# Kernel tuning notes

Hardware: AMD Instinct MI355X
Metric: run time of the kernel (lower is better)

Reference implementation:

```python
import jax, jax.numpy as jnp
import numpy as np
from jax import lax

B, T, D = 2, 2048, 2048
H, DK, DV = 16, 128, 128
K = 4  # conv kernel size
KEY_DIM = H * DK      # 2048
VAL_DIM = H * DV      # 2048
CONV_DIM = 2 * KEY_DIM + VAL_DIM  # 6144
EPS = 1e-6


def setup_inputs() -> dict:
    key = jax.random.key(0)
    ks = jax.random.split(key, 10)
    s = lambda fan: 1.0 / np.sqrt(fan)
    return {
        "hidden_states": jax.random.normal(ks[0], (B, T, D), jnp.float32),
        "W_qkv": jax.random.normal(ks[1], (D, CONV_DIM), jnp.float32) * s(D),
        "conv_w": jax.random.normal(ks[2], (CONV_DIM, 1, K), jnp.float32) * s(K),
        "W_z": jax.random.normal(ks[3], (D, VAL_DIM), jnp.float32) * s(D),
        "W_b": jax.random.normal(ks[4], (D, H), jnp.float32) * s(D),
        "W_a": jax.random.normal(ks[5], (D, H), jnp.float32) * s(D),
        "dt_bias": jnp.ones((H,), jnp.float32),
        "A_log": jnp.log(jax.random.uniform(ks[6], (H,), jnp.float32, 1e-3, 16.0)),
        "norm_weight": jnp.ones((DV,), jnp.float32),
        "W_out": jax.random.normal(ks[7], (VAL_DIM, D), jnp.float32) * s(VAL_DIM),
    }


def _l2norm(x):
    return x * lax.rsqrt(jnp.sum(x * x, axis=-1, keepdims=True) + 1e-6)


def _gated_delta_rule(q, k, v, g, beta):
    """q,k: [B,T,H,DK]; v: [B,T,H,DV]; g,beta: [B,T,H]. Returns o: [B,T,H,DV]."""
    # time-major for scan
    qT, kT, vT = (jnp.moveaxis(x, 1, 0) for x in (q, k, v))  # [T,B,H,d]
    gT = jnp.moveaxis(g, 1, 0)      # [T,B,H]
    bT = jnp.moveaxis(beta, 1, 0)   # [T,B,H]

    def step(S, inp):
        q_t, k_t, v_t, g_t, b_t = inp
        S = S * jnp.exp(g_t)[..., None, None]                      # decay [B,H,DK,DV]
        kv_mem = jnp.einsum("bhk,bhkv->bhv", k_t, S)               # S^T k
        delta = (v_t - kv_mem) * b_t[..., None]                     # beta-scaled error
        S = S + jnp.einsum("bhk,bhv->bhkv", k_t, delta)
        o_t = jnp.einsum("bhk,bhkv->bhv", q_t, S)
        return S, o_t

    S0 = jnp.zeros((q.shape[0], H, DK, DV), q.dtype)
    _, oT = lax.scan(step, S0, (qT, kT, vT, gT, bT))
    return jnp.moveaxis(oT, 0, 1)  # [B,T,H,DV]


def reference(hidden_states, W_qkv, conv_w, W_z, W_b, W_a, dt_bias, A_log,
              norm_weight, W_out):
    Bs, Ts, _ = hidden_states.shape

    # qkv projection + depthwise causal conv1d + silu
    mixed = hidden_states @ W_qkv                      # [B,T,CONV_DIM]
    xc = jnp.moveaxis(mixed, 1, 2)                     # [B,C,T]
    xc = lax.conv_general_dilated(xc, conv_w, (1,), [(K - 1, 0)],
                                  feature_group_count=CONV_DIM)
    mixed = jax.nn.silu(jnp.moveaxis(xc, 1, 2))        # [B,T,C]

    q, k, v = jnp.split(mixed, [KEY_DIM, 2 * KEY_DIM], axis=-1)
    q = _l2norm(q.reshape(Bs, Ts, H, DK)) * (DK ** -0.5)
    k = _l2norm(k.reshape(Bs, Ts, H, DK))
    v = v.reshape(Bs, Ts, H, DV)

    beta = jax.nn.sigmoid(hidden_states @ W_b)                     # [B,T,H]
    g = -jnp.exp(A_log) * jax.nn.softplus(hidden_states @ W_a + dt_bias)

    o = _gated_delta_rule(q, k, v, g, beta)            # [B,T,H,DV]

    # gated RMSNorm (Mamba2-style: gate first, then normalize)
    z = (hidden_states @ W_z).reshape(Bs, Ts, H, DV)
    o = o * jax.nn.silu(z)
    var = jnp.mean(o * o, axis=-1, keepdims=True)
    o = o * lax.rsqrt(var + EPS) * norm_weight

    return o.reshape(Bs, Ts, VAL_DIM) @ W_out          # [B,T,D]
```

## Files before the change

kernel.cpp:

```cpp
#include <hip/hip_runtime.h>

#define B_ 2
#define T_ 2048
#define D_ 2048
#define H_ 16
#define CONV_DIM_ 6144
#define NC_ 32
#define CK_ 64

typedef __bf16 bf16;
typedef bf16 bf16x8 __attribute__((ext_vector_type(8)));
typedef bf16 bf16x4 __attribute__((ext_vector_type(4)));
typedef float floatx4 __attribute__((ext_vector_type(4)));

__device__ __forceinline__ void async_copy16(bf16* lds, const bf16* g) {
    auto* g1 = (const __attribute__((address_space(1))) unsigned int*)g;
    auto* l3 = (__attribute__((address_space(3))) unsigned int*)lds;
    __builtin_amdgcn_global_load_lds(g1, l3, 16, 0, 0);
}

__global__ void cvt_bf16_kernel(const float* __restrict__ in, bf16* __restrict__ out, int n4) {
    int i = blockIdx.x * 256 + threadIdx.x;
    if (i < n4) {
        float4 v = ((const float4*)in)[i];
        bf16x4 o = { (bf16)v.x, (bf16)v.y, (bf16)v.z, (bf16)v.w };
        *(bf16x4*)(out + 4 * (size_t)i) = o;
    }
}

__global__ void transpose_kernel(const float* __restrict__ in, bf16* __restrict__ out, int R, int Cn) {
    __shared__ float tile[32][33];
    const int c0 = blockIdx.x << 5, r0 = blockIdx.y << 5;
    const int tx = threadIdx.x & 31, ty = threadIdx.x >> 5;
#pragma unroll
    for (int i = 0; i < 4; ++i) {
        int r = ty + (i << 3);
        tile[r][tx] = in[(size_t)(r0 + r) * Cn + c0 + tx];
    }
    __syncthreads();
#pragma unroll
    for (int i = 0; i < 4; ++i) {
        int cc = ty + (i << 3);
        out[(size_t)(c0 + cc) * R + r0 + tx] = (bf16)tile[tx][cc];
    }
}

__global__ void wba_cvt_kernel(const float* __restrict__ Wb, const float* __restrict__ Wa,
                               bf16* __restrict__ Wba) {
    int idx = blockIdx.x * 256 + threadIdx.x;
    int d = idx >> 4, h = idx & 15;
    Wba[(size_t)h * 2048 + d]        = (bf16)Wb[idx];
    Wba[(size_t)(h + 16) * 2048 + d] = (bf16)Wa[idx];
}

template <typename OutT>
__global__ __launch_bounds__(256) void gemm_kernel(
    const bf16* __restrict__ A, const bf16* __restrict__ Bt, OutT* __restrict__ C,
    int M, int N, int K) {
    __shared__ bf16 As[128 * 64];
    __shared__ bf16 Bs[128 * 64];
    const int tid = threadIdx.x;
    const int m0 = blockIdx.y << 7;
    const int n0 = blockIdx.x << 7;
    const int wave = tid >> 6, lane = tid & 63;
    const int wm = (wave >> 1) << 6, wn = (wave & 1) << 6;
    const int lrow = lane & 15, quad = lane >> 4;
    const int rl = lane >> 3;
    const int c8s = (lane & 7) ^ (rl & 7);

    floatx4 acc[4][4];
#pragma unroll
    for (int mt = 0; mt < 4; ++mt)
#pragma unroll
        for (int nt = 0; nt < 4; ++nt)
            acc[mt][nt] = floatx4{0.f, 0.f, 0.f, 0.f};

    for (int k0 = 0; k0 < K; k0 += 64) {
        __syncthreads();
#pragma unroll
        for (int i = 0; i < 4; ++i) {
            const int slot = wave * 4 + i;
            const int r = slot * 8 + rl;
            async_copy16(&As[slot * 512], A + (size_t)(m0 + r) * K + k0 + c8s * 8);
            async_copy16(&Bs[slot * 512], Bt + (size_t)(n0 + r) * K + k0 + c8s * 8);
        }
        __syncthreads();
#pragma unroll
        for (int kk = 0; kk < 64; kk += 32) {
            const int sw = (((kk >> 3) + quad) ^ (lrow & 7)) << 3;
            bf16x8 af[4], bfr[4];
#pragma unroll
            for (int mt = 0; mt < 4; ++mt) {
                af[mt]  = *(const bf16x8*)(&As[((wm + (mt << 4) + lrow) << 6) + sw]);
                bfr[mt] = *(const bf16x8*)(&Bs[((wn + (mt << 4) + lrow) << 6) + sw]);
            }
#pragma unroll
            for (int mt = 0; mt < 4; ++mt)
#pragma unroll
                for (int nt = 0; nt < 4; ++nt)
                    acc[mt][nt] = __builtin_amdgcn_mfma_f32_16x16x32_bf16(af[mt], bfr[nt], acc[mt][nt], 0, 0, 0);
        }
    }
#pragma unroll
    for (int mt = 0; mt < 4; ++mt)
#pragma unroll
        for (int nt = 0; nt < 4; ++nt) {
            const int col = n0 + wn + (nt << 4) + lrow;
            const int rowb = m0 + wm + (mt << 4) + (quad << 2);
#pragma unroll
            for (int i2 = 0; i2 < 4; ++i2)
                C[(size_t)(rowb + i2) * N + col] = (OutT)acc[mt][nt][i2];
        }
}

__global__ __launch_bounds__(512, 2) void gemm256_kernel(
    const bf16* __restrict__ A, const bf16* __restrict__ Bt,
    bf16* __restrict__ C0, bf16* __restrict__ C1,
    int M, int Ncat, int K, int split, int ld0, int ld1) {
    __shared__ bf16 As[4][256 * 32];
    __shared__ bf16 Bs[4][256 * 32];
    const int tid = threadIdx.x;
    const int wave = tid >> 6, lane = tid & 63;
    const int quad = lane >> 4, lrow = lane & 15;
    const int wm = (wave >> 2) << 7;
    const int wn = (wave & 3) << 6;
    const int orig = blockIdx.y * gridDim.x + blockIdx.x;
    const int xcd = orig & 7, pos = orig >> 3;
    const int nblk = (xcd << 2) | (pos >> 4);
    const int mblk = pos & 15;
    const int m0 = mblk << 8, n0 = nblk << 8;

    const bf16* gA[2];
    const bf16* gB[2];
#pragma unroll
    for (int i = 0; i < 2; ++i) {
        const int q = wave * 2 + i;
        const int u = (lane & 7) ^ (lane >> 3);
        const int row = (q * 8 + (lane >> 3)) * 2 + (u >> 2);
        const int col = (u & 3) * 8;
        gA[i] = A  + (size_t)(m0 + row) * K + col;
        gB[i] = Bt + (size_t)(n0 + row) * K + col;
    }

    auto loff = [](int row, int qd) -> int {
        return ((row >> 1) << 6) + (((((row & 1) << 2) | qd) ^ ((row >> 1) & 7)) << 3);
    };

    floatx4 acc[8][4];
#pragma unroll
    for (int mt = 0; mt < 8; ++mt)
#pragma unroll
        for (int nt = 0; nt < 4; ++nt)
            acc[mt][nt] = floatx4{0.f, 0.f, 0.f, 0.f};

    const int KT = K >> 5;

#pragma unroll
    for (int t = 0; t < 3; ++t) {
        async_copy16(&As[t][(wave * 2 + 0) * 512], gA[0] + t * 32);
        async_copy16(&As[t][(wave * 2 + 1) * 512], gA[1] + t * 32);
        async_copy16(&Bs[t][(wave * 2 + 0) * 512], gB[0] + t * 32);
        async_copy16(&Bs[t][(wave * 2 + 1) * 512], gB[1] + t * 32);
    }
    asm volatile("s_waitcnt vmcnt(8)" ::: "memory");
    __builtin_amdgcn_s_barrier();

    for (int t = 0; t < KT; ++t) {
        const int b = t & 3;
        const bf16* as = &As[b][0];
        const bf16* bs = &Bs[b][0];
        bf16x8 bfr[4], af[4];
#pragma unroll
        for (int nt = 0; nt < 4; ++nt)
            bfr[nt] = *(const bf16x8*)(bs + loff(wn + nt * 16 + lrow, quad));
#pragma unroll
        for (int mt = 0; mt < 4; ++mt)
            af[mt] = *(const bf16x8*)(as + loff(wm + mt * 16 + lrow, quad));
        if (t + 2 < KT)       asm volatile("s_waitcnt vmcnt(4)" ::: "memory");
        else if (t + 2 == KT) asm volatile("s_waitcnt vmcnt(0)" ::: "memory");
        if (t + 3 < KT) {
            const int bn = (t + 3) & 3;
            async_copy16(&As[bn][(wave * 2 + 0) * 512], gA[0] + (t + 3) * 32);
            async_copy16(&As[bn][(wave * 2 + 1) * 512], gA[1] + (t + 3) * 32);
        }
        __builtin_amdgcn_s_barrier();
        asm volatile("s_waitcnt lgkmcnt(0)" ::: "memory");
        __builtin_amdgcn_sched_barrier(0);
        __builtin_amdgcn_s_setprio(1);
#pragma unroll
        for (int mt = 0; mt < 4; ++mt)
#pragma unroll
            for (int nt = 0; nt < 4; ++nt)
                acc[mt][nt] = __builtin_amdgcn_mfma_f32_16x16x32_bf16(
                    af[mt], bfr[nt], acc[mt][nt], 0, 0, 0);
        __builtin_amdgcn_s_setprio(0);
        __builtin_amdgcn_sched_barrier(0);
        __builtin_amdgcn_s_barrier();
#pragma unroll
        for (int mt = 0; mt < 4; ++mt)
            af[mt] = *(const bf16x8*)(as + loff(wm + 64 + mt * 16 + lrow, quad));
        if (t + 3 < KT) {
            const int bn = (t + 3) & 3;
            async_copy16(&Bs[bn][(wave * 2 + 0) * 512], gB[0] + (t + 3) * 32);
            async_copy16(&Bs[bn][(wave * 2 + 1) * 512], gB[1] + (t + 3) * 32);
        }
        __builtin_amdgcn_s_barrier();
        asm volatile("s_waitcnt lgkmcnt(0)" ::: "memory");
        __builtin_amdgcn_sched_barrier(0);
        __builtin_amdgcn_s_setprio(1);
#pragma unroll
        for (int mt = 0; mt < 4; ++mt)
#pragma unroll
            for (int nt = 0; nt < 4; ++nt)
                acc[4 + mt][nt] = __builtin_amdgcn_mfma_f32_16x16x32_bf16(
                    af[mt], bfr[nt], acc[4 + mt][nt], 0, 0, 0);
        __builtin_amdgcn_s_setprio(0);
        __builtin_amdgcn_sched_barrier(0);
        __builtin_amdgcn_s_barrier();
    }

    const bool second = (n0 >= split);
    bf16* Cp = second ? C1 : C0;
    const int ldc = second ? ld1 : ld0;
    const int nc0 = second ? n0 - split : n0;
#pragma unroll
    for (int mt = 0; mt < 8; ++mt)
#pragma unroll
        for (int nt = 0; nt < 4; ++nt) {
            const int col = nc0 + wn + nt * 16 + lrow;
            const int rowb = m0 + wm + mt * 16 + (quad << 2);
#pragma unroll
            for (int i2 = 0; i2 < 4; ++i2)
                Cp[(size_t)(rowb + i2) * ldc + col] = (bf16)acc[mt][nt][i2];
        }
}

__global__ __launch_bounds__(256) void conv_silu_kernel(
    const bf16* __restrict__ mixed, const float* __restrict__ cw,
    bf16* __restrict__ qb, bf16* __restrict__ kb, bf16* __restrict__ vb) {
    const int bt = blockIdx.y;
    const int t = bt & (T_ - 1);
    const int b = bt >> 11;
    const int c0 = blockIdx.x * 2048 + threadIdx.x * 8;
    const size_t base = (size_t)bt * CONV_DIM_ + c0;

    bf16x8 zz;
#pragma unroll
    for (int j = 0; j < 8; ++j) zz[j] = (bf16)0.f;
    const bf16x8 r3 = *(const bf16x8*)(mixed + base);
    const bf16x8 r2 = (t >= 1) ? *(const bf16x8*)(mixed + base - CONV_DIM_) : zz;
    const bf16x8 r1 = (t >= 2) ? *(const bf16x8*)(mixed + base - 2 * CONV_DIM_) : zz;
    const bf16x8 r0 = (t >= 3) ? *(const bf16x8*)(mixed + base - 3 * CONV_DIM_) : zz;

    const float4* cw4 = (const float4*)cw;
    float vals[8];
    float ss = 0.f;
#pragma unroll
    for (int j = 0; j < 8; ++j) {
        const float4 w = cw4[c0 + j];
        float acc = (float)r3[j] * w.w + (float)r2[j] * w.z +
                    (float)r1[j] * w.y + (float)r0[j] * w.x;
        const float sv = acc / (1.f + __expf(-acc));
        vals[j] = sv;
        ss += sv * sv;
    }

    if (c0 < 4096) {
#pragma unroll
        for (int o = 1; o < 16; o <<= 1) ss += __shfl_xor(ss, o);
        const float scale = rsqrtf(ss + 1e-6f);
        const bool isq = c0 < 2048;
        const float mul = isq ? scale * 0.08838834764831845f : scale;
        const int h = (c0 >> 7) & 15;
        const int d0 = c0 & 127;
        const size_t oidx = (((size_t)(b * H_ + h)) * T_ + t) * 128 + d0;
        bf16x8 o8;
#pragma unroll
        for (int j = 0; j < 8; ++j) o8[j] = (bf16)(vals[j] * mul);
        *(bf16x8*)((isq ? qb : kb) + oidx) = o8;
    } else {
        const int h = (c0 >> 7) & 15;
        const int d0 = c0 & 127;
        const size_t oidx = (((size_t)(b * H_ + h)) * T_ + t) * 128 + d0;
        bf16x8 o8;
#pragma unroll
        for (int j = 0; j < 8; ++j) o8[j] = (bf16)vals[j];
        *(bf16x8*)(vb + oidx) = o8;
    }
}

__global__ __launch_bounds__(256) void gbeta_mfma_kernel(
    const bf16* __restrict__ Xb, const bf16* __restrict__ Wba,
    const float* __restrict__ dtb, const float* __restrict__ Alog,
    float* __restrict__ gbuf, float* __restrict__ bbuf) {
    const int tid = threadIdx.x, wave = tid >> 6, lane = tid & 63;
    const int ln = lane & 15, qd = lane >> 4;
    const int m0 = blockIdx.x * 64 + wave * 16;
    floatx4 acc0 = {0.f, 0.f, 0.f, 0.f}, acc1 = {0.f, 0.f, 0.f, 0.f};
    const bf16* arow = Xb + (size_t)(m0 + ln) * 2048 + qd * 8;
    const bf16* b0 = Wba + (size_t)ln * 2048 + qd * 8;
    const bf16* b1 = Wba + (size_t)(16 + ln) * 2048 + qd * 8;
    for (int k = 0; k < 2048; k += 32) {
        bf16x8 af  = *(const bf16x8*)(arow + k);
        bf16x8 bf0 = *(const bf16x8*)(b0 + k);
        bf16x8 bf1 = *(const bf16x8*)(b1 + k);
        acc0 = __builtin_amdgcn_mfma_f32_16x16x32_bf16(af, bf0, acc0, 0, 0, 0);
        acc1 = __builtin_amdgcn_mfma_f32_16x16x32_bf16(af, bf1, acc1, 0, 0, 0);
    }
    const float dtbv = dtb[ln], al = __expf(Alog[ln]);
#pragma unroll
    for (int ii = 0; ii < 4; ++ii) {
        const int row = m0 + qd * 4 + ii;
        const int t = row & (T_ - 1), b = row >> 11;
        const size_t o = ((size_t)(b * H_ + ln)) * T_ + t;
        bbuf[o] = 1.f / (1.f + __expf(-acc0[ii]));
        const float xx = acc1[ii] + dtbv;
        const float sp = (xx > 15.f) ? xx : log1pf(__expf(xx));
        gbuf[o] = -al * sp;
    }
}

__global__ __launch_bounds__(256) void qkkt_kernel(const bf16* __restrict__ qb, const bf16* __restrict__ kb,
                                                   float* __restrict__ Araw, float* __restrict__ Mraw) {
    const int u = blockIdx.x;
    const int bh = u >> 5, nc = u & 31;
    const int t0 = nc * CK_;
    const int tid = threadIdx.x, wave = tid >> 6, lane = tid & 63;
    const int qd = lane >> 4, ln = lane & 15;
    __shared__ bf16 Kc[64 * 136], Qc[64 * 136];
    const size_t kbase = ((size_t)bh * T_ + t0) * 128;
#pragma unroll
    for (int it = 0; it < 4; ++it) {
        int idx = it * 256 + tid;
        int row = idx >> 4, c8 = idx & 15;
        *(uint4*)(&Kc[row * 136 + c8 * 8]) = *(const uint4*)(kb + kbase + row * 128 + c8 * 8);
        *(uint4*)(&Qc[row * 136 + c8 * 8]) = *(const uint4*)(qb + kbase + row * 128 + c8 * 8);
    }
    __syncthreads();
#pragma unroll
    for (int nt = 0; nt < 4; ++nt) {
        floatx4 accA = {0.f, 0.f, 0.f, 0.f}, accM = {0.f, 0.f, 0.f, 0.f};
#pragma unroll
        for (int kk = 0; kk < 4; ++kk) {
            bf16x8 bfr = *(const bf16x8*)(&Kc[(nt * 16 + ln) * 136 + kk * 32 + qd * 8]);
            bf16x8 afK = *(const bf16x8*)(&Kc[(wave * 16 + ln) * 136 + kk * 32 + qd * 8]);
            bf16x8 afQ = *(const bf16x8*)(&Qc[(wave * 16 + ln) * 136 + kk * 32 + qd * 8]);
            accA = __builtin_amdgcn_mfma_f32_16x16x32_bf16(afK, bfr, accA, 0, 0, 0);
            accM = __builtin_amdgcn_mfma_f32_16x16x32_bf16(afQ, bfr, accM, 0, 0, 0);
        }
#pragma unroll
        for (int ii = 0; ii < 4; ++ii) {
            int i = wave * 16 + qd * 4 + ii, j = nt * 16 + ln;
            Araw[(size_t)u * 4096 + i * 64 + j] = accA[ii];
            Mraw[(size_t)u * 4096 + i * 64 + j] = accM[ii];
        }
    }
}

__global__ __launch_bounds__(64) void prep_kernel(
    const float* __restrict__ gbuf, const float* __restrict__ bbuf,
    const float* __restrict__ Araw, const float* __restrict__ Mraw,
    float* __restrict__ lamg, float* __restrict__ ratiog,
    bf16* __restrict__ Tg, bf16* __restrict__ Mg) {
    const int u = blockIdx.x, bh = u >> 5, nc = u & 31, t0 = nc * CK_;
    const int lane = threadIdx.x;
    __shared__ float L[64 * 65];
    __shared__ float cv[64], bv[64];
    float g = gbuf[(size_t)bh * T_ + t0 + lane];
    float beta = bbuf[(size_t)bh * T_ + t0 + lane];
    float c = g;
#pragma unroll
    for (int off = 1; off < 64; off <<= 1) {
        float tval = __shfl_up(c, off);
        if (lane >= off) c += tval;
    }
    float c63 = __shfl(c, 63);
    lamg[(size_t)u * 64 + lane] = __expf(c);
    ratiog[(size_t)u * 64 + lane] = __expf(c63 - c);
    cv[lane] = c; bv[lane] = beta;
    __syncthreads();
    for (int i = 0; i < 64; ++i) {
        float a = Araw[(size_t)u * 4096 + i * 64 + lane];
        L[i * 65 + lane] = (lane < i) ? bv[i] * __expf(cv[i] - c) * a : 0.f;
    }
    __syncthreads();
    float t[64];
#pragma unroll
    for (int i = 0; i < 64; ++i) t[i] = (i == lane) ? 1.f : 0.f;
#pragma unroll
    for (int j = 0; j < 63; ++j) {
#pragma unroll
        for (int i = j + 1; i < 64; ++i)
            t[i] -= L[i * 65 + j] * t[j];
    }
#pragma unroll
    for (int i = 0; i < 64; ++i)
        Tg[(size_t)u * 4096 + i * 64 + lane] = (bf16)t[i];
    for (int i = 0; i < 64; ++i) {
        float m = Mraw[(size_t)u * 4096 + i * 64 + lane];
        float mij = (lane <= i) ? __expf(cv[i] - c) * m : 0.f;
        Mg[(size_t)u * 4096 + i * 64 + lane] = (bf16)mij;
    }
}

struct Pref {
    uint4 t2[2], m2[2];
    bf16x8 kf[4], qf[4];
    bf16x8 ktf[2][2];
    float rrv[4], vv[4], lam[4], bet[4], lamlast;
};

__device__ __forceinline__ void load_pref(
    Pref& p, int u, int t0, size_t kbase, int tid, int wave, int ln, int qd,
    int bh, int vbase,
    const bf16* __restrict__ qb, const bf16* __restrict__ kb, const bf16* __restrict__ vb,
    const bf16* __restrict__ Tg, const bf16* __restrict__ Mg,
    const float* __restrict__ lamg, const float* __restrict__ ratiog,
    const float* __restrict__ bbuf) {
#pragma unroll
    for (int it = 0; it < 2; ++it) {
        int idx = it * 256 + tid;
        int row = idx >> 3, c8 = idx & 7;
        p.t2[it] = *(const uint4*)(Tg + (size_t)u * 4096 + row * 64 + c8 * 8);
        p.m2[it] = *(const uint4*)(Mg + (size_t)u * 4096 + row * 64 + c8 * 8);
    }
    const size_t rowoff = kbase + (size_t)(wave * 16 + ln) * 128;
#pragma unroll
    for (int kk = 0; kk < 4; ++kk) {
        p.kf[kk] = *(const bf16x8*)(kb + rowoff + kk * 32 + qd * 8);
        p.qf[kk] = *(const bf16x8*)(qb + rowoff + kk * 32 + qd * 8);
    }
    const int i0 = wave * 16 + qd * 4;
#pragma unroll
    for (int ii = 0; ii < 4; ++ii) {
        p.vv[ii]  = (float)vb[kbase + (size_t)(i0 + ii) * 128 + vbase + ln];
        p.lam[ii] = lamg[(size_t)u * 64 + i0 + ii];
        p.bet[ii] = bbuf[(size_t)bh * T_ + t0 + i0 + ii];
        p.rrv[ii] = ratiog[(size_t)u * 64 + i0 + ii];
    }
    p.lamlast = lamg[(size_t)u * 64 + 63];
#pragma unroll
    for (int mt = 0; mt < 2; ++mt) {
        const int kd = (wave * 2 + mt) * 16 + ln;
#pragma unroll
        for (int kk2 = 0; kk2 < 2; ++kk2) {
            const int ib = kk2 * 32 + qd * 8;
#pragma unroll
            for (int j = 0; j < 8; ++j)
                p.ktf[mt][kk2][j] = kb[kbase + (size_t)(ib + j) * 128 + kd];
        }
    }
}

__global__ __launch_bounds__(256) void seq_kernel(
    const bf16* __restrict__ qb, const bf16* __restrict__ kb, const bf16* __restrict__ vb,
    const bf16* __restrict__ Tg, const bf16* __restrict__ Mg,
    const float* __restrict__ lamg, const float* __restrict__ ratiog,
    const float* __restrict__ bbuf, float* __restrict__ ob) {
    const int bh = blockIdx.x & 31;
    const int vs = blockIdx.x >> 5;
    const int vbase = vs * 16;
    const int tid = threadIdx.x;
    const int wave = tid >> 6, lane = tid & 63;
    const int qd = lane >> 4, ln = lane & 15;

    __shared__ bf16 Tt[64 * 72], Mm[64 * 72];
    __shared__ bf16 bT[16 * 72], Dt[16 * 72], Dtr[16 * 72];
    __shared__ bf16 Sbf[16 * 136];
    __shared__ float Sf[16 * 132];

    for (int idx = tid; idx < 16 * 132; idx += 256) Sf[idx] = 0.f;
    for (int idx = tid; idx < 16 * 136; idx += 256) Sbf[idx] = (bf16)0.f;

    auto chunk_body = [&](Pref& cur, Pref& nxt, int nc) {
        const int t0 = nc * CK_;
        const size_t kbase = ((size_t)bh * T_ + t0) * 128;

#pragma unroll
        for (int it = 0; it < 2; ++it) {
            int idx = it * 256 + tid;
            int row = idx >> 3, c8 = idx & 7;
            *(uint4*)(&Tt[row * 72 + c8 * 8]) = cur.t2[it];
            *(uint4*)(&Mm[row * 72 + c8 * 8]) = cur.m2[it];
        }

        {
            const int ncn = (nc + 1 < NC_) ? nc + 1 : nc;
            load_pref(nxt, bh * NC_ + ncn, ncn * CK_, ((size_t)bh * T_ + (size_t)ncn * CK_) * 128,
                      tid, wave, ln, qd, bh, vbase, qb, kb, vb, Tg, Mg, lamg, ratiog, bbuf);
        }

        floatx4 ks = {0.f, 0.f, 0.f, 0.f};
#pragma unroll
        for (int kk = 0; kk < 4; ++kk) {
            bf16x8 bf = *(const bf16x8*)(&Sbf[ln * 136 + kk * 32 + qd * 8]);
            ks = __builtin_amdgcn_mfma_f32_16x16x32_bf16(cur.kf[kk], bf, ks, 0, 0, 0);
        }
        {
            const int i0 = wave * 16 + qd * 4;
            bf16x4 bw;
#pragma unroll
            for (int ii = 0; ii < 4; ++ii)
                bw[ii] = (bf16)(cur.bet[ii] * (cur.vv[ii] - cur.lam[ii] * ks[ii]));
            *(bf16x4*)(&bT[ln * 72 + i0]) = bw;
        }
        __syncthreads();

        {
            floatx4 acc = {0.f, 0.f, 0.f, 0.f};
#pragma unroll
            for (int kk = 0; kk < 2; ++kk) {
                bf16x8 af = *(const bf16x8*)(&Tt[(wave * 16 + ln) * 72 + kk * 32 + qd * 8]);
                bf16x8 bf = *(const bf16x8*)(&bT[ln * 72 + kk * 32 + qd * 8]);
                acc = __builtin_amdgcn_mfma_f32_16x16x32_bf16(af, bf, acc, 0, 0, 0);
            }
            const int i0 = wave * 16 + qd * 4;
            bf16x4 dw = { (bf16)acc[0], (bf16)acc[1], (bf16)acc[2], (bf16)acc[3] };
            *(bf16x4*)(&Dt[ln * 72 + i0]) = dw;
            bf16x4 dwr = { (bf16)(acc[0] * cur.rrv[0]), (bf16)(acc[1] * cur.rrv[1]),
                           (bf16)(acc[2] * cur.rrv[2]), (bf16)(acc[3] * cur.rrv[3]) };
            *(bf16x4*)(&Dtr[ln * 72 + i0]) = dwr;
        }
        __syncthreads();

        {
            floatx4 acc = {0.f, 0.f, 0.f, 0.f};
#pragma unroll
            for (int kk = 0; kk < 4; ++kk) {
                bf16x8 bf = *(const bf16x8*)(&Sbf[ln * 136 + kk * 32 + qd * 8]);
                acc = __builtin_amdgcn_mfma_f32_16x16x32_bf16(cur.qf[kk], bf, acc, 0, 0, 0);
            }
            floatx4 o;
#pragma unroll
            for (int ii = 0; ii < 4; ++ii) o[ii] = acc[ii] * cur.lam[ii];
#pragma unroll
            for (int kk = 0; kk < 2; ++kk) {
                bf16x8 af = *(const bf16x8*)(&Mm[(wave * 16 + ln) * 72 + kk * 32 + qd * 8]);
                bf16x8 bf = *(const bf16x8*)(&Dt[ln * 72 + kk * 32 + qd * 8]);
                o = __builtin_amdgcn_mfma_f32_16x16x32_bf16(af, bf, o, 0, 0, 0);
            }
            const int i0 = wave * 16 + qd * 4;
#pragma unroll
            for (int ii = 0; ii < 4; ++ii)
                ob[kbase + (size_t)(i0 + ii) * 128 + vbase + ln] = o[ii];
        }
#pragma unroll
        for (int mt = 0; mt < 2; ++mt) {
            const int kt = wave * 2 + mt;
            floatx4 acc = {0.f, 0.f, 0.f, 0.f};
#pragma unroll
            for (int kk = 0; kk < 2; ++kk) {
                bf16x8 bf = *(const bf16x8*)(&Dtr[ln * 72 + kk * 32 + qd * 8]);
                acc = __builtin_amdgcn_mfma_f32_16x16x32_bf16(cur.ktf[mt][kk], bf, acc, 0, 0, 0);
            }
            const int k0 = kt * 16 + qd * 4;
            floatx4 sold = *(floatx4*)(&Sf[ln * 132 + k0]);
#pragma unroll
            for (int ii = 0; ii < 4; ++ii) sold[ii] = sold[ii] * cur.lamlast + acc[ii];
            *(floatx4*)(&Sf[ln * 132 + k0]) = sold;
        }
        __syncthreads();
        {
            const int vloc = tid >> 4, k0 = (tid & 15) * 8;
            floatx4 s0 = *(floatx4*)(&Sf[vloc * 132 + k0]);
            floatx4 s1 = *(floatx4*)(&Sf[vloc * 132 + k0 + 4]);
            bf16x8 sb = { (bf16)s0[0], (bf16)s0[1], (bf16)s0[2], (bf16)s0[3],
                          (bf16)s1[0], (bf16)s1[1], (bf16)s1[2], (bf16)s1[3] };
            *(bf16x8*)(&Sbf[vloc * 136 + k0]) = sb;
        }
        __syncthreads();
    };

    Pref pA, pB;
    load_pref(pA, bh * NC_, 0, (size_t)bh * T_ * 128, tid, wave, ln, qd, bh, vbase,
              qb, kb, vb, Tg, Mg, lamg, ratiog, bbuf);
    __syncthreads();

#pragma unroll 1
    for (int nc2 = 0; nc2 < NC_; nc2 += 2) {
        chunk_body(pA, pB, nc2);
        chunk_body(pB, pA, nc2 + 1);
    }
}

__global__ void gated_norm_kernel(const float* __restrict__ ob, const bf16* __restrict__ z,
                                  const float* __restrict__ nw, bf16* __restrict__ onorm) {
    const int idx = blockIdx.x;
    const int h = idx & (H_ - 1);
    const int bt = idx >> 4;
    const int t = bt & (T_ - 1);
    const int b = bt >> 11;
    const int tid = threadIdx.x;
    const size_t obase = (((size_t)(b * H_ + h)) * T_ + t) * 128;
    const size_t zbase = (size_t)bt * 2048 + (h << 7);
    float o1 = ob[obase + tid], o2 = ob[obase + tid + 64];
    const float z1 = (float)z[zbase + tid], z2 = (float)z[zbase + tid + 64];
    o1 *= z1 / (1.f + __expf(-z1));
    o2 *= z2 / (1.f + __expf(-z2));
    float ss = o1 * o1 + o2 * o2;
#pragma unroll
    for (int o = 1; o < 64; o <<= 1) ss += __shfl_xor(ss, o);
    const float scale = rsqrtf(ss * (1.f / 128.f) + 1e-6f);
    onorm[zbase + tid]      = (bf16)(o1 * scale * nw[tid]);
    onorm[zbase + tid + 64] = (bf16)(o2 * scale * nw[tid + 64]);
}

extern "C" void kernel_launch(void* const* d_in, const int* in_sizes, int n_in,
                              void* d_out, int out_size, void* d_ws, size_t ws_size,
                              hipStream_t stream) {
    const float* X    = (const float*)d_in[0];
    const float* Wqkv = (const float*)d_in[1];
    const float* cw   = (const float*)d_in[2];
    const float* Wz   = (const float*)d_in[3];
    const float* Wb   = (const float*)d_in[4];
    const float* Wa   = (const float*)d_in[5];
    const float* dtb  = (const float*)d_in[6];
    const float* Alog = (const float*)d_in[7];
    const float* nw   = (const float*)d_in[8];
    const float* Wout = (const float*)d_in[9];
    float* out = (float*)d_out;

    char* ws = (char*)d_ws;
    size_t off = 0;
    auto alloc = [&](size_t bytes) -> char* {
        char* p = ws + off;
        off += (bytes + 255) & ~(size_t)255;
        return p;
    };
    bf16*  Xb      = (bf16*)alloc((size_t)B_ * T_ * D_ * 2);
    char*  wcat_p  = alloc((size_t)8192 * 2048 * 2);
    bf16*  Wcat    = (bf16*)wcat_p;
    bf16*  Woutt   = (bf16*)alloc((size_t)D_ * D_ * 2);
    bf16*  Wba     = (bf16*)alloc((size_t)32 * 2048 * 2);
    char*  mixed_p = alloc((size_t)B_ * T_ * CONV_DIM_ * 2);
    bf16*  mixedb  = (bf16*)mixed_p;
    bf16*  zb      = (bf16*)alloc((size_t)B_ * T_ * D_ * 2);
    bf16*  kbuf    = (bf16*)alloc((size_t)B_ * T_ * D_ * 2);
    bf16*  vbuf    = (bf16*)alloc((size_t)B_ * T_ * D_ * 2);
    float* gbuf    = (float*)alloc((size_t)B_ * T_ * H_ * 4);
    float* bbuf    = (float*)alloc((size_t)B_ * T_ * H_ * 4);
    float* Mraw    = (float*)alloc((size_t)1024 * 4096 * 4);
    bf16*  Tg      = (bf16*)alloc((size_t)1024 * 4096 * 2);
    bf16*  Mg      = (bf16*)alloc((size_t)1024 * 4096 * 2);
    float* lamg    = (float*)alloc((size_t)1024 * 64 * 4);
    float* ratiog  = (float*)alloc((size_t)1024 * 64 * 4);
    bf16*  qbuf    = (bf16*)wcat_p;
    float* obuf    = (float*)mixed_p;
    float* Araw    = (float*)(mixed_p + (size_t)B_ * T_ * D_ * 4);
    bf16*  onorm   = (bf16*)Xb;

    cvt_bf16_kernel<<<dim3((B_ * T_ * D_ / 4 + 255) / 256), dim3(256), 0, stream>>>(X, Xb, B_ * T_ * D_ / 4);
    transpose_kernel<<<dim3(CONV_DIM_ / 32, D_ / 32), dim3(256), 0, stream>>>(Wqkv, Wcat, D_, CONV_DIM_);
    transpose_kernel<<<dim3(D_ / 32, D_ / 32), dim3(256), 0, stream>>>(Wz, Wcat + (size_t)CONV_DIM_ * D_, D_, D_);
    transpose_kernel<<<dim3(D_ / 32, D_ / 32), dim3(256), 0, stream>>>(Wout, Woutt, D_, D_);
    wba_cvt_kernel<<<dim3(128), dim3(256), 0, stream>>>(Wb, Wa, Wba);

    gemm256_kernel<<<dim3(8192 / 256, B_ * T_ / 256), dim3(512), 0, stream>>>(
        Xb, Wcat, mixedb, zb, B_ * T_, 8192, D_, CONV_DIM_, CONV_DIM_, D_);

    gbeta_mfma_kernel<<<dim3(64), dim3(256), 0, stream>>>(Xb, Wba, dtb, Alog, gbuf, bbuf);
    conv_silu_kernel<<<dim3(CONV_DIM_ / 2048, B_ * T_), dim3(256), 0, stream>>>(mixedb, cw, qbuf, kbuf, vbuf);

    qkkt_kernel<<<dim3(1024), dim3(256), 0, stream>>>(qbuf, kbuf, Araw, Mraw);
    prep_kernel<<<dim3(1024), dim3(64), 0, stream>>>(gbuf, bbuf, Araw, Mraw, lamg, ratiog, Tg, Mg);
    seq_kernel<<<dim3(256), dim3(256), 0, stream>>>(qbuf, kbuf, vbuf, Tg, Mg, lamg, ratiog, bbuf, obuf);

    gated_norm_kernel<<<dim3(B_ * T_ * H_), dim3(64), 0, stream>>>(obuf, zb, nw, onorm);

    gemm_kernel<float><<<dim3(D_ / 128, B_ * T_ / 128), dim3(256), 0, stream>>>(
        onorm, Woutt, out, B_ * T_, D_, D_);
}
```

Measured before the change: 608.0 us.

## Keep chunk state in registers with double-buffered bf16 copy; drop GEMM XCD remap

The fp32 recurrent state in the sequential delta-rule kernel now lives in per-thread registers instead of LDS. Each thread writes its bf16 copy straight into a ping-pong LDS buffer, which removes one __syncthreads and the separate fp32-to-bf16 conversion pass per chunk. The GEMM kernel also drops its XCD-aware block remapping in favour of plain blockIdx tiling. That change may reduce L2 locality across chiplets.

Result: no change. 602.4 us (-0.9%).

```diff
diff --git a/kernel.cpp b/kernel.cpp
--- a/kernel.cpp
+++ b/kernel.cpp
@@ -124,11 +124,7 @@
     const int quad = lane >> 4, lrow = lane & 15;
     const int wm = (wave >> 2) << 7;
     const int wn = (wave & 3) << 6;
-    const int orig = blockIdx.y * gridDim.x + blockIdx.x;
-    const int xcd = orig & 7, pos = orig >> 3;
-    const int nblk = (xcd << 2) | (pos >> 4);
-    const int mblk = pos & 15;
-    const int m0 = mblk << 8, n0 = nblk << 8;
+    const int m0 = blockIdx.y << 8, n0 = blockIdx.x << 8;
 
     const bf16* gA[2];
     const bf16* gB[2];
@@ -466,13 +462,14 @@
 
     __shared__ bf16 Tt[64 * 72], Mm[64 * 72];
     __shared__ bf16 bT[16 * 72], Dt[16 * 72], Dtr[16 * 72];
-    __shared__ bf16 Sbf[16 * 136];
-    __shared__ float Sf[16 * 132];
-
-    for (int idx = tid; idx < 16 * 132; idx += 256) Sf[idx] = 0.f;
-    for (int idx = tid; idx < 16 * 136; idx += 256) Sbf[idx] = (bf16)0.f;
-
-    auto chunk_body = [&](Pref& cur, Pref& nxt, int nc) {
+    __shared__ bf16 Sbf[2][16 * 136];
+
+    for (int idx = tid; idx < 2 * 16 * 136; idx += 256)
+        (&Sbf[0][0])[idx] = (bf16)0.f;
+
+    floatx4 Sreg[2] = { floatx4{0.f, 0.f, 0.f, 0.f}, floatx4{0.f, 0.f, 0.f, 0.f} };
+
+    auto chunk_body = [&](Pref& cur, Pref& nxt, int nc, bf16* Srd, bf16* Swr) {
         const int t0 = nc * CK_;
         const size_t kbase = ((size_t)bh * T_ + t0) * 128;
 
@@ -493,7 +490,7 @@
         floatx4 ks = {0.f, 0.f, 0.f, 0.f};
 #pragma unroll
         for (int kk = 0; kk < 4; ++kk) {
-            bf16x8 bf = *(const bf16x8*)(&Sbf[ln * 136 + kk * 32 + qd * 8]);
+            bf16x8 bf = *(const bf16x8*)(&Srd[ln * 136 + kk * 32 + qd * 8]);
             ks = __builtin_amdgcn_mfma_f32_16x16x32_bf16(cur.kf[kk], bf, ks, 0, 0, 0);
         }
         {
@@ -527,7 +524,7 @@
             floatx4 acc = {0.f, 0.f, 0.f, 0.f};
 #pragma unroll
             for (int kk = 0; kk < 4; ++kk) {
-                bf16x8 bf = *(const bf16x8*)(&Sbf[ln * 136 + kk * 32 + qd * 8]);
+                bf16x8 bf = *(const bf16x8*)(&Srd[ln * 136 + kk * 32 + qd * 8]);
                 acc = __builtin_amdgcn_mfma_f32_16x16x32_bf16(cur.qf[kk], bf, acc, 0, 0, 0);
             }
             floatx4 o;
@@ -553,20 +550,12 @@
                 bf16x8 bf = *(const bf16x8*)(&Dtr[ln * 72 + kk * 32 + qd * 8]);
                 acc = __builtin_amdgcn_mfma_f32_16x16x32_bf16(cur.ktf[mt][kk], bf, acc, 0, 0, 0);
             }
-            const int k0 = kt * 16 + qd * 4;
-            floatx4 sold = *(floatx4*)(&Sf[ln * 132 + k0]);
+            floatx4 sold = Sreg[mt];
 #pragma unroll
             for (int ii = 0; ii < 4; ++ii) sold[ii] = sold[ii] * cur.lamlast + acc[ii];
-            *(floatx4*)(&Sf[ln * 132 + k0]) = sold;
-        }
-        __syncthreads();
-        {
-            const int vloc = tid >> 4, k0 = (tid & 15) * 8;
-            floatx4 s0 = *(floatx4*)(&Sf[vloc * 132 + k0]);
-            floatx4 s1 = *(floatx4*)(&Sf[vloc * 132 + k0 + 4]);
-            bf16x8 sb = { (bf16)s0[0], (bf16)s0[1], (bf16)s0[2], (bf16)s0[3],
-                          (bf16)s1[0], (bf16)s1[1], (bf16)s1[2], (bf16)s1[3] };
-            *(bf16x8*)(&Sbf[vloc * 136 + k0]) = sb;
+            Sreg[mt] = sold;
+            bf16x4 sb4 = { (bf16)sold[0], (bf16)sold[1], (bf16)sold[2], (bf16)sold[3] };
+            *(bf16x4*)(&Swr[ln * 136 + kt * 16 + qd * 4]) = sb4;
         }
         __syncthreads();
     };
@@ -578,8 +567,8 @@
 
 #pragma unroll 1
     for (int nc2 = 0; nc2 < NC_; nc2 += 2) {
-        chunk_body(pA, pB, nc2);
-        chunk_body(pB, pA, nc2 + 1);
+        chunk_body(pA, pB, nc2,     &Sbf[0][0], &Sbf[1][0]);
+        chunk_body(pB, pA, nc2 + 1, &Sbf[1][0], &Sbf[0][0]);
     }
 }
 
```
